# Kernel optimization log

Measured on AMD Instinct MI355X. Metric: run time of the kernel, lower is better.

The kernel has to match this reference:

```python
import jax, jax.numpy as jnp
import numpy as np

NUM_HEADS = 16
CLAMP = 1e4


def setup_inputs() -> dict:
    key = jax.random.key(0)
    ks = jax.random.split(key, 8)
    B, Nq, Nkv, Cq, Ckv = 4, 2048, 2048, 1024, 768
    s_q = 1.0 / np.sqrt(Cq)
    s_kv = 1.0 / np.sqrt(Ckv)
    return {
        "query": jax.random.normal(ks[0], (B, Nq, Cq), jnp.float32),
        "key_value": jax.random.normal(ks[1], (B, Nkv, Ckv), jnp.float32),
        "Wq": jax.random.normal(ks[2], (Cq, Cq), jnp.float32) * s_q,
        "bq": jnp.zeros((Cq,), jnp.float32),
        "Wk": jax.random.normal(ks[3], (Ckv, Cq), jnp.float32) * s_kv,
        "bk": jnp.zeros((Cq,), jnp.float32),
        "Wv": jax.random.normal(ks[4], (Ckv, Cq), jnp.float32) * s_kv,
        "bv": jnp.zeros((Cq,), jnp.float32),
        "Wo": jax.random.normal(ks[5], (Cq, Cq), jnp.float32) * s_q,
        "bo": jnp.zeros((Cq,), jnp.float32),
    }


def reference(query, key_value, Wq, bq, Wk, bk, Wv, bv, Wo, bo):
    B, Nq, Cq = query.shape
    Nkv = key_value.shape[1]
    H = NUM_HEADS
    D = Cq // H
    scale = D ** (-0.5)

    # projections -> [B, H, N, D]
    q = (query @ Wq + bq).reshape(B, Nq, H, D).transpose(0, 2, 1, 3)
    k = (key_value @ Wk + bk).reshape(B, Nkv, H, D).transpose(0, 2, 1, 3)
    v = (key_value @ Wv + bv).reshape(B, Nkv, H, D).transpose(0, 2, 1, 3)

    # scores [B, H, Nq, Nkv] with clamp (mask=None path)
    attn = jnp.einsum("bhqd,bhkd->bhqk", q, k) * scale
    attn = jnp.clip(attn, -CLAMP, CLAMP)
    attn = jax.nn.softmax(attn, axis=-1)
    # NaN fallback: replace with uniform attention if any NaN present
    attn = jnp.where(jnp.any(jnp.isnan(attn)),
                     jnp.asarray(1.0 / Nkv, attn.dtype), attn)

    # weighted sum -> [B, Nq, Cq]
    x = jnp.einsum("bhqk,bhkd->bqhd", attn, v).reshape(B, Nq, Cq)
    return x @ Wo + bo
```

## Files before the change

### kernel.cpp

```cpp
#include <hip/hip_runtime.h>
#include <hip/hip_bf16.h>
#include <stdint.h>


typedef unsigned short u16;
typedef __attribute__((ext_vector_type(4))) short bf16x4;
typedef __attribute__((ext_vector_type(8))) short bf16x8;
typedef __attribute__((ext_vector_type(4))) float f32x4;
typedef __attribute__((ext_vector_type(16))) float f32x16;

__device__ __forceinline__ u16 f2bf(float x) {
  union { float f; uint32_t u; } c; c.f = x;
  uint32_t r = c.u + 0x7fffu + ((c.u >> 16) & 1u);
  return (u16)(r >> 16);
}

__device__ __forceinline__ uint32_t pkbf(float a, float b) {
#if __has_builtin(__builtin_amdgcn_cvt_pk_bf16_f32)
  typedef __attribute__((ext_vector_type(2))) __bf16 bf2;
  bf2 r = __builtin_amdgcn_cvt_pk_bf16_f32(a, b);
  return __builtin_bit_cast(uint32_t, r);
#else
  return (uint32_t)f2bf(a) | ((uint32_t)f2bf(b) << 16);
#endif
}

__device__ __forceinline__ void gld16(const void* g, void* l) {
  __builtin_amdgcn_global_load_lds(
      (const __attribute__((address_space(1))) void*)g,
      (__attribute__((address_space(3))) void*)l, 16, 0, 0);
}

__device__ __forceinline__ void cvt_body(const float* __restrict__ in,
                                         u16* __restrict__ out, int blk) {
  int i = (blk * 256 + threadIdx.x) * 8;
  float4 a = *(const float4*)(in + i);
  float4 b = *(const float4*)(in + i + 4);
  union { u16 u[8]; uint4 v; } o;
  o.u[0] = f2bf(a.x); o.u[1] = f2bf(a.y); o.u[2] = f2bf(a.z); o.u[3] = f2bf(a.w);
  o.u[4] = f2bf(b.x); o.u[5] = f2bf(b.y); o.u[6] = f2bf(b.z); o.u[7] = f2bf(b.w);
  *(uint4*)(out + i) = o.v;
}

__device__ __forceinline__ void transpose_body(const float* __restrict__ in,
                                               u16* __restrict__ out,
                                               int R, int C, int bx, int by) {
  __shared__ float tile[64][65];
  int c0 = bx * 64, r0 = by * 64;
  #pragma unroll
  for (int it = 0; it < 16; it++) {
    int idx = threadIdx.x + it * 256;
    int lr = idx >> 6, lc = idx & 63;
    tile[lr][lc] = in[(size_t)(r0 + lr) * C + c0 + lc];
  }
  __syncthreads();
  #pragma unroll
  for (int it = 0; it < 16; it++) {
    int idx = threadIdx.x + it * 256;
    int lc = idx >> 6, lr = idx & 63;
    out[(size_t)(c0 + lc) * R + r0 + lr] = f2bf(tile[lr][lc]);
  }
}

__global__ void prep_kernel(const float* __restrict__ query,
                            const float* __restrict__ key_value,
                            const float* __restrict__ Wq, const float* __restrict__ Wk,
                            const float* __restrict__ Wv, const float* __restrict__ Wo,
                            u16* qb, u16* kvb, u16* WqT, u16* WkT, u16* WvT, u16* WoT) {
  int blk = blockIdx.x;
  if (blk < 4096) { cvt_body(query, qb, blk); return; }
  if (blk < 7168) { cvt_body(key_value, kvb, blk - 4096); return; }
  if (blk < 7424) { int lo = blk - 7168; transpose_body(Wq, WqT, 1024, 1024, lo & 15, lo >> 4); return; }
  if (blk < 7616) { int lo = blk - 7424; transpose_body(Wk, WkT, 768, 1024, lo & 15, lo >> 4); return; }
  if (blk < 7808) { int lo = blk - 7616; transpose_body(Wv, WvT, 768, 1024, lo & 15, lo >> 4); return; }
  { int lo = blk - 7808; transpose_body(Wo, WoT, 1024, 1024, lo & 15, lo >> 4); return; }
}

template<bool SWAP>
__device__ __forceinline__ void gemm_kloop(const u16* __restrict__ A,
                                           const u16* __restrict__ BT,
                                           int K, char* smem, f32x4 (&acc)[4][4],
                                           int m0, int n0, int tid) {
  const u16* ap[4]; const u16* bp[4]; int ldA[4], ldB[4];
  #pragma unroll
  for (int it2 = 0; it2 < 4; it2++) {
    int s = it2 * 256 + tid;
    int row = s >> 3, cl = (s & 7) ^ (row & 7);
    ap[it2] = A + (size_t)(m0 + row) * K + cl * 8;
    bp[it2] = BT + (size_t)(n0 + row) * K + cl * 8;
    ldA[it2] = s * 16;
    ldB[it2] = 16384 + s * 16;
  }
  const int w = tid >> 6, l = tid & 63;
  const int lm = l & 15, lq = l >> 4;
  const int wr = w >> 1, wc = w & 1;
  int abase[4], bbase[4];
  #pragma unroll
  for (int i = 0; i < 4; i++) {
    int m = wr * 64 + i * 16 + lm;
    abase[i] = m * 128 + ((lq ^ (m & 7)) << 4);
    int n = wc * 64 + i * 16 + lm;
    bbase[i] = 16384 + n * 128 + ((lq ^ (n & 7)) << 4);
  }
  for (int k0 = 0; k0 < K; k0 += 64) {
    #pragma unroll
    for (int it2 = 0; it2 < 4; it2++) {
      gld16(ap[it2], smem + ldA[it2]);
      gld16(bp[it2], smem + ldB[it2]);
      ap[it2] += 64; bp[it2] += 64;
    }
    __syncthreads();
    #pragma unroll
    for (int kk = 0; kk < 2; kk++) {
      bf16x8 af[4], bf[4];
      #pragma unroll
      for (int i = 0; i < 4; i++)
        af[i] = *(const bf16x8*)(smem + (abase[i] ^ (kk << 6)));
      #pragma unroll
      for (int j = 0; j < 4; j++)
        bf[j] = *(const bf16x8*)(smem + (bbase[j] ^ (kk << 6)));
      #pragma unroll
      for (int i = 0; i < 4; i++)
        #pragma unroll
        for (int j = 0; j < 4; j++) {
          if (SWAP)
            acc[i][j] = __builtin_amdgcn_mfma_f32_16x16x32_bf16(bf[j], af[i], acc[i][j], 0, 0, 0);
          else
            acc[i][j] = __builtin_amdgcn_mfma_f32_16x16x32_bf16(af[i], bf[j], acc[i][j], 0, 0, 0);
        }
    }
    __syncthreads();
  }
}

__global__ __launch_bounds__(256, 2)
void gemm_qkv(const u16* __restrict__ qb, const u16* __restrict__ kvb,
              const u16* __restrict__ WqT, const u16* __restrict__ WkT,
              const u16* __restrict__ WvT,
              const float* __restrict__ bq, const float* __restrict__ bk,
              const float* __restrict__ bv,
              u16* __restrict__ Qb, u16* __restrict__ Kbf, u16* __restrict__ Vt,
              float qscale) {
  extern __shared__ __align__(16) char smem[];
  const int tid = threadIdx.x;
  const int w = tid >> 6, l = tid & 63;
  const int lm = l & 15, lq = l >> 4;
  const int m0 = blockIdx.y * 128, n0 = blockIdx.x * 128;
  const int wr = w >> 1, wc = w & 1;
  const int z = blockIdx.z;
  f32x4 acc[4][4] = {};

  u16* etile = (u16*)(smem + w * 9216);
  const int xr = l >> 3, cc = (l & 7) ^ xr;

  if (z < 2) {
    const u16* A = (z == 0) ? qb : kvb;
    const u16* BT = (z == 0) ? WqT : WkT;
    const float* bias = (z == 0) ? bq : bk;
    u16* out = (z == 0) ? Qb : Kbf;
    const float scale = (z == 0) ? qscale : 1.0f;
    const int K = (z == 0) ? 1024 : 768;
    gemm_kloop<true>(A, BT, K, smem, acc, m0, n0, tid);
    #pragma unroll
    for (int j = 0; j < 4; j++) {
      float4 b4 = *(const float4*)&bias[n0 + wc * 64 + j * 16 + lq * 4];
      #pragma unroll
      for (int i = 0; i < 4; i++) {
        uint2 pkd;
        pkd.x = pkbf((acc[i][j][0] + b4.x) * scale, (acc[i][j][1] + b4.y) * scale);
        pkd.y = pkbf((acc[i][j][2] + b4.z) * scale, (acc[i][j][3] + b4.w) * scale);
        *(uint2*)&etile[(i * 16 + lm) * 72 + j * 16 + lq * 4] = pkd;
      }
    }
    u16* gbase = out + (size_t)(m0 + wr * 64) * 1024 + n0 + wc * 64;
    #pragma unroll
    for (int co = 0; co < 8; co++) {
      int ml = co * 8 + xr;
      uint4 d = *(const uint4*)&etile[ml * 72 + cc * 8];
      *(uint4*)&gbase[(size_t)ml * 1024 + cc * 8] = d;
    }
  } else {
    gemm_kloop<false>(kvb, WvT, 768, smem, acc, m0, n0, tid);
    #pragma unroll
    for (int j = 0; j < 4; j++) {
      float bi = bv[n0 + wc * 64 + j * 16 + lm];
      #pragma unroll
      for (int i = 0; i < 4; i++) {
        uint2 pkd;
        pkd.x = pkbf(acc[i][j][0] + bi, acc[i][j][1] + bi);
        pkd.y = pkbf(acc[i][j][2] + bi, acc[i][j][3] + bi);
        *(uint2*)&etile[(j * 16 + lm) * 72 + i * 16 + lq * 4] = pkd;
      }
    }
    const int bb = m0 >> 11, mloc = (m0 & 2047) + wr * 64;
    u16* gbase = Vt + ((size_t)bb * 1024 + n0 + wc * 64) * 2048 + mloc;
    const int kvA = (cc >> 1) * 16 + (cc & 1) * 4;
    #pragma unroll
    for (int co = 0; co < 8; co++) {
      int dl = co * 8 + xr;
      uint2 dA = *(const uint2*)&etile[dl * 72 + kvA];
      uint2 dB = *(const uint2*)&etile[dl * 72 + kvA + 8];
      uint4 d = {dA.x, dA.y, dB.x, dB.y};
      *(uint4*)&gbase[(size_t)dl * 2048 + cc * 8] = d;
    }
  }
}

__global__ __launch_bounds__(256, 2)
void gemm_o(const u16* __restrict__ A, const u16* __restrict__ BT,
            const float* __restrict__ bias, float* __restrict__ Cout) {
  __shared__ __align__(16) char smem[32768];
  const int tid = threadIdx.x;
  const int w = tid >> 6, l = tid & 63;
  const int lm = l & 15, lq = l >> 4;
  const int m0 = blockIdx.y * 128, n0 = blockIdx.x * 128;
  const int wr = w >> 1, wc = w & 1;
  f32x4 acc[4][4] = {};
  gemm_kloop<false>(A, BT, 1024, smem, acc, m0, n0, tid);
  #pragma unroll
  for (int j = 0; j < 4; j++) {
    int gn = n0 + wc * 64 + j * 16 + lm;
    float bi = bias[gn];
    #pragma unroll
    for (int i = 0; i < 4; i++) {
      int gm = m0 + wr * 64 + i * 16 + lq * 4;
      #pragma unroll
      for (int r = 0; r < 4; r++)
        Cout[(size_t)(gm + r) * 1024 + gn] = acc[i][j][r] + bi;
    }
  }
}

__global__ __launch_bounds__(256, 3)
void attn_kernel(const u16* __restrict__ Q, const u16* __restrict__ Kb,
                 const u16* __restrict__ Vt, u16* __restrict__ X) {
  __shared__ __align__(16) char smem[32768];
  const int tid = threadIdx.x, w = tid >> 6, l = tid & 63;
  const int l31 = l & 31, h5 = l >> 5;
  const int bh = blockIdx.x, b = bh >> 4, h = bh & 15;
  const int q0 = blockIdx.y * 128 + w * 32;
  const int rx = l31 & 7;

  const u16* Kg = Kb + (size_t)b * 2048 * 1024 + h * 64;
  const u16* Vg = Vt + (size_t)bh * 64 * 2048;

  const u16 *kp0, *kp1, *vp0, *vp1;
  {
    int s = tid, r = s >> 3, c = (s & 7) ^ (r & 7);
    kp0 = Kg + (size_t)r * 1024 + c * 8;
    vp0 = Vg + (size_t)r * 2048 + c * 8;
    s = 256 + tid; r = s >> 3; c = (s & 7) ^ (r & 7);
    kp1 = Kg + (size_t)r * 1024 + c * 8;
    vp1 = Vg + (size_t)r * 2048 + c * 8;
  }
  const int kd0 = tid * 16, kd1 = (256 + tid) * 16;

  bf16x8 qf[4];
  {
    const u16* qp = Q + ((size_t)(b * 2048 + q0 + l31)) * 1024 + h * 64 + h5 * 8;
    #pragma unroll
    for (int t = 0; t < 4; t++) qf[t] = *(const bf16x8*)(qp + t * 16);
  }

  const int kvb2 = (l31 << 7) | ((rx ^ h5) << 4);
  const int vb2 = 16384 | (l31 << 7) | ((rx ^ h5) << 4);

  f32x16 xacc[2] = {};
  f32x4 ls4 = {0.f, 0.f, 0.f, 0.f};
  const f32x16 KZ = {};

  gld16(kp0, smem + kd0); gld16(kp1, smem + kd1);
  gld16(vp0, smem + 16384 + kd0); gld16(vp1, smem + 16384 + kd1);
  kp0 += 65536; kp1 += 65536; vp0 += 64; vp1 += 64;
  __syncthreads();

#define ATTN_STEP(CUR, DOPREF)                                                  \
  {                                                                             \
    if (DOPREF) {                                                               \
      const int nb = ((CUR) ^ 1) << 13;                                         \
      gld16(kp0, smem + nb + kd0); gld16(kp1, smem + nb + kd1);                 \
      gld16(vp0, smem + 16384 + nb + kd0); gld16(vp1, smem + 16384 + nb + kd1); \
      kp0 += 65536; kp1 += 65536; vp0 += 64; vp1 += 64;                         \
    }                                                                           \
    _Pragma("unroll")                                                           \
    for (int sub = 0; sub < 2; sub++) {                                         \
      const int km = ((CUR) << 13) | (sub << 12);                               \
      bf16x8 kf = *(const bf16x8*)(smem + (kvb2 ^ km));                         \
      f32x16 st = __builtin_amdgcn_mfma_f32_32x32x16_bf16(kf, qf[0], KZ, 0, 0, 0); \
      _Pragma("unroll")                                                         \
      for (int t = 1; t < 4; t++) {                                             \
        kf = *(const bf16x8*)(smem + (kvb2 ^ (km | (t << 5))));                 \
        st = __builtin_amdgcn_mfma_f32_32x32x16_bf16(kf, qf[t], st, 0, 0, 0);   \
      }                                                                         \
      float p[16];                                                              \
      _Pragma("unroll")                                                         \
      for (int r = 0; r < 16; r++) p[r] = __builtin_amdgcn_exp2f(st[r]);        \
      _Pragma("unroll")                                                         \
      for (int u = 0; u < 4; u++)                                               \
        ls4[u] += (p[4 * u] + p[4 * u + 1]) + (p[4 * u + 2] + p[4 * u + 3]);    \
      uint32_t pk[8];                                                           \
      _Pragma("unroll")                                                         \
      for (int qd = 0; qd < 8; qd++) pk[qd] = pkbf(p[2 * qd], p[2 * qd + 1]);   \
      _Pragma("unroll")                                                         \
      for (int c2 = 0; c2 < 2; c2++) {                                          \
        union { uint32_t d[4]; bf16x8 v; } pf;                                  \
        pf.d[0] = pk[4 * c2 + 0]; pf.d[1] = pk[4 * c2 + 1];                     \
        pf.d[2] = pk[4 * c2 + 2]; pf.d[3] = pk[4 * c2 + 3];                     \
        const int vx = ((sub << 2) | (c2 << 1)) << 4;                           \
        _Pragma("unroll")                                                       \
        for (int dt = 0; dt < 2; dt++) {                                        \
          bf16x8 vf = *(const bf16x8*)(smem +                                   \
              (vb2 ^ (((CUR) << 13) | (dt << 12) | vx)));                       \
          xacc[dt] = __builtin_amdgcn_mfma_f32_32x32x16_bf16(vf, pf.v, xacc[dt], 0, 0, 0); \
        }                                                                       \
      }                                                                         \
    }                                                                           \
    __syncthreads();                                                            \
  }

  for (int itp = 0; itp < 15; itp++) {
    ATTN_STEP(0, true)
    ATTN_STEP(1, true)
  }
  ATTN_STEP(0, true)
  ATTN_STEP(1, false)
#undef ATTN_STEP

  float lsum = (ls4[0] + ls4[1]) + (ls4[2] + ls4[3]);
  const float inv = 1.0f / (lsum + __shfl_xor(lsum, 32));
  u16* xp = X + ((size_t)(b * 2048 + q0 + l31)) * 1024 + h * 64;
  #pragma unroll
  for (int dt = 0; dt < 2; dt++)
    #pragma unroll
    for (int g = 0; g < 4; g++) {
      const int d0 = dt * 32 + g * 8 + h5 * 4;
      uint2 o;
      o.x = pkbf(xacc[dt][4 * g + 0] * inv, xacc[dt][4 * g + 1] * inv);
      o.y = pkbf(xacc[dt][4 * g + 2] * inv, xacc[dt][4 * g + 3] * inv);
      *(uint2*)(xp + d0) = o;
    }
}

extern "C" void kernel_launch(void* const* d_in, const int* in_sizes, int n_in,
                              void* d_out, int out_size, void* d_ws, size_t ws_size,
                              hipStream_t stream) {
  const float* query     = (const float*)d_in[0];
  const float* key_value = (const float*)d_in[1];
  const float* Wq = (const float*)d_in[2];
  const float* bq = (const float*)d_in[3];
  const float* Wk = (const float*)d_in[4];
  const float* bk = (const float*)d_in[5];
  const float* Wv = (const float*)d_in[6];
  const float* bv = (const float*)d_in[7];
  const float* Wo = (const float*)d_in[8];
  const float* bo = (const float*)d_in[9];
  float* out = (float*)d_out;

  char* ws = (char*)d_ws;
  size_t off = 0;
  auto alloc = [&](size_t bytes) -> void* {
    void* p = ws + off; off += (bytes + 255) & ~(size_t)255; return p;
  };
  u16* qb  = (u16*)alloc((size_t)8192 * 1024 * 2);
  u16* kvb = (u16*)alloc((size_t)8192 * 768 * 2);
  u16* WqT = (u16*)alloc((size_t)1024 * 1024 * 2);
  u16* WkT = (u16*)alloc((size_t)1024 * 768 * 2);
  u16* WvT = (u16*)alloc((size_t)1024 * 768 * 2);
  u16* WoT = (u16*)alloc((size_t)1024 * 1024 * 2);
  u16* Qb  = (u16*)alloc((size_t)8192 * 1024 * 2);
  u16* Kbf = (u16*)alloc((size_t)8192 * 1024 * 2);
  u16* Vt  = (u16*)alloc((size_t)8192 * 1024 * 2);
  u16* Xb  = (u16*)alloc((size_t)8192 * 1024 * 2);

  prep_kernel<<<8064, 256, 0, stream>>>(query, key_value, Wq, Wk, Wv, Wo,
                                        qb, kvb, WqT, WkT, WvT, WoT);

  const float qscale = 0.125f * 1.4426950408889634f;
  gemm_qkv<<<dim3(8, 64, 3), 256, 36864, stream>>>(qb, kvb, WqT, WkT, WvT,
                                                   bq, bk, bv, Qb, Kbf, Vt, qscale);

  attn_kernel<<<dim3(64, 16), 256, 0, stream>>>(Qb, Kbf, Vt, Xb);

  gemm_o<<<dim3(8, 64), 256, 0, stream>>>(Xb, WoT, bo, out);
}
```

Measured before the change: 293.1 us.

## Process two query tiles per wave in attention to reuse K/V fragments

Each attention wave now handles 64 query rows, as two 32-row tiles, instead of 32. K and V fragments loaded from LDS are reused across both tiles, and the grid is halved. This cuts LDS and global K/V traffic per query and gives more independent MFMA work to interleave. The cost is higher register pressure, so attention occupancy drops to 2 blocks per CU while the GEMM kernels' launch bounds are raised to 3.

Measured after the change: 291.0 us. No clear change (-0.7%).

```diff
diff --git a/kernel.cpp b/kernel.cpp
--- a/kernel.cpp
+++ b/kernel.cpp
@@ -4,6 +4,7 @@
 
 
 typedef unsigned short u16;
+typedef __attribute__((ext_vector_type(2))) float f32x2;
 typedef __attribute__((ext_vector_type(4))) short bf16x4;
 typedef __attribute__((ext_vector_type(8))) short bf16x8;
 typedef __attribute__((ext_vector_type(4))) float f32x4;
@@ -133,7 +134,7 @@
   }
 }
 
-__global__ __launch_bounds__(256, 2)
+__global__ __launch_bounds__(256, 3)
 void gemm_qkv(const u16* __restrict__ qb, const u16* __restrict__ kvb,
               const u16* __restrict__ WqT, const u16* __restrict__ WkT,
               const u16* __restrict__ WvT,
@@ -206,7 +207,7 @@
   }
 }
 
-__global__ __launch_bounds__(256, 2)
+__global__ __launch_bounds__(256, 3)
 void gemm_o(const u16* __restrict__ A, const u16* __restrict__ BT,
             const float* __restrict__ bias, float* __restrict__ Cout) {
   __shared__ __align__(16) char smem[32768];
@@ -231,14 +232,14 @@
   }
 }
 
-__global__ __launch_bounds__(256, 3)
+__global__ __launch_bounds__(256, 2)
 void attn_kernel(const u16* __restrict__ Q, const u16* __restrict__ Kb,
                  const u16* __restrict__ Vt, u16* __restrict__ X) {
   __shared__ __align__(16) char smem[32768];
   const int tid = threadIdx.x, w = tid >> 6, l = tid & 63;
   const int l31 = l & 31, h5 = l >> 5;
   const int bh = blockIdx.x, b = bh >> 4, h = bh & 15;
-  const int q0 = blockIdx.y * 128 + w * 32;
+  const int q0 = blockIdx.y * 256 + w * 64;
   const int rx = l31 & 7;
 
   const u16* Kg = Kb + (size_t)b * 2048 * 1024 + h * 64;
@@ -255,18 +256,21 @@
   }
   const int kd0 = tid * 16, kd1 = (256 + tid) * 16;
 
-  bf16x8 qf[4];
+  bf16x8 qfA[4], qfB[4];
   {
     const u16* qp = Q + ((size_t)(b * 2048 + q0 + l31)) * 1024 + h * 64 + h5 * 8;
     #pragma unroll
-    for (int t = 0; t < 4; t++) qf[t] = *(const bf16x8*)(qp + t * 16);
+    for (int t = 0; t < 4; t++) qfA[t] = *(const bf16x8*)(qp + t * 16);
+    qp += (size_t)32 * 1024;
+    #pragma unroll
+    for (int t = 0; t < 4; t++) qfB[t] = *(const bf16x8*)(qp + t * 16);
   }
 
   const int kvb2 = (l31 << 7) | ((rx ^ h5) << 4);
   const int vb2 = 16384 | (l31 << 7) | ((rx ^ h5) << 4);
 
-  f32x16 xacc[2] = {};
-  f32x4 ls4 = {0.f, 0.f, 0.f, 0.f};
+  f32x16 xaccA[2] = {}, xaccB[2] = {};
+  f32x2 lsA = {0.f, 0.f}, lsB = {0.f, 0.f};
   const f32x16 KZ = {};
 
   gld16(kp0, smem + kd0); gld16(kp1, smem + kd1);
@@ -285,33 +289,51 @@
     _Pragma("unroll")                                                           \
     for (int sub = 0; sub < 2; sub++) {                                         \
       const int km = ((CUR) << 13) | (sub << 12);                               \
-      bf16x8 kf = *(const bf16x8*)(smem + (kvb2 ^ km));                         \
-      f32x16 st = __builtin_amdgcn_mfma_f32_32x32x16_bf16(kf, qf[0], KZ, 0, 0, 0); \
-      _Pragma("unroll")                                                         \
-      for (int t = 1; t < 4; t++) {                                             \
-        kf = *(const bf16x8*)(smem + (kvb2 ^ (km | (t << 5))));                 \
-        st = __builtin_amdgcn_mfma_f32_32x32x16_bf16(kf, qf[t], st, 0, 0, 0);   \
+      bf16x8 kf[4];                                                             \
+      _Pragma("unroll")                                                         \
+      for (int t = 0; t < 4; t++)                                               \
+        kf[t] = *(const bf16x8*)(smem + (kvb2 ^ (km | (t << 5))));              \
+      f32x16 st = __builtin_amdgcn_mfma_f32_32x32x16_bf16(kf[0], qfA[0], KZ, 0, 0, 0); \
+      _Pragma("unroll")                                                         \
+      for (int t = 1; t < 4; t++)                                               \
+        st = __builtin_amdgcn_mfma_f32_32x32x16_bf16(kf[t], qfA[t], st, 0, 0, 0); \
+      uint32_t pkA[8], pkB[8];                                                  \
+      _Pragma("unroll")                                                         \
+      for (int u = 0; u < 4; u++) {                                             \
+        float p0 = __builtin_amdgcn_exp2f(st[4 * u + 0]);                       \
+        float p1 = __builtin_amdgcn_exp2f(st[4 * u + 1]);                       \
+        float p2 = __builtin_amdgcn_exp2f(st[4 * u + 2]);                       \
+        float p3 = __builtin_amdgcn_exp2f(st[4 * u + 3]);                       \
+        lsA += (f32x2){p0 + p2, p1 + p3};                                       \
+        pkA[2 * u] = pkbf(p0, p1); pkA[2 * u + 1] = pkbf(p2, p3);               \
       }                                                                         \
-      float p[16];                                                              \
-      _Pragma("unroll")                                                         \
-      for (int r = 0; r < 16; r++) p[r] = __builtin_amdgcn_exp2f(st[r]);        \
-      _Pragma("unroll")                                                         \
-      for (int u = 0; u < 4; u++)                                               \
-        ls4[u] += (p[4 * u] + p[4 * u + 1]) + (p[4 * u + 2] + p[4 * u + 3]);    \
-      uint32_t pk[8];                                                           \
-      _Pragma("unroll")                                                         \
-      for (int qd = 0; qd < 8; qd++) pk[qd] = pkbf(p[2 * qd], p[2 * qd + 1]);   \
+      st = __builtin_amdgcn_mfma_f32_32x32x16_bf16(kf[0], qfB[0], KZ, 0, 0, 0); \
+      _Pragma("unroll")                                                         \
+      for (int t = 1; t < 4; t++)                                               \
+        st = __builtin_amdgcn_mfma_f32_32x32x16_bf16(kf[t], qfB[t], st, 0, 0, 0); \
+      _Pragma("unroll")                                                         \
+      for (int u = 0; u < 4; u++) {                                             \
+        float p0 = __builtin_amdgcn_exp2f(st[4 * u + 0]);                       \
+        float p1 = __builtin_amdgcn_exp2f(st[4 * u + 1]);                       \
+        float p2 = __builtin_amdgcn_exp2f(st[4 * u + 2]);                       \
+        float p3 = __builtin_amdgcn_exp2f(st[4 * u + 3]);                       \
+        lsB += (f32x2){p0 + p2, p1 + p3};                                       \
+        pkB[2 * u] = pkbf(p0, p1); pkB[2 * u + 1] = pkbf(p2, p3);               \
+      }                                                                         \
       _Pragma("unroll")                                                         \
       for (int c2 = 0; c2 < 2; c2++) {                                          \
-        union { uint32_t d[4]; bf16x8 v; } pf;                                  \
-        pf.d[0] = pk[4 * c2 + 0]; pf.d[1] = pk[4 * c2 + 1];                     \
-        pf.d[2] = pk[4 * c2 + 2]; pf.d[3] = pk[4 * c2 + 3];                     \
+        union { uint32_t d[4]; bf16x8 v; } pfA, pfB;                            \
+        _Pragma("unroll")                                                       \
+        for (int dd = 0; dd < 4; dd++) {                                        \
+          pfA.d[dd] = pkA[4 * c2 + dd]; pfB.d[dd] = pkB[4 * c2 + dd];           \
+        }                                                                       \
         const int vx = ((sub << 2) | (c2 << 1)) << 4;                           \
         _Pragma("unroll")                                                       \
         for (int dt = 0; dt < 2; dt++) {                                        \
           bf16x8 vf = *(const bf16x8*)(smem +                                   \
               (vb2 ^ (((CUR) << 13) | (dt << 12) | vx)));                       \
-          xacc[dt] = __builtin_amdgcn_mfma_f32_32x32x16_bf16(vf, pf.v, xacc[dt], 0, 0, 0); \
+          xaccA[dt] = __builtin_amdgcn_mfma_f32_32x32x16_bf16(vf, pfA.v, xaccA[dt], 0, 0, 0); \
+          xaccB[dt] = __builtin_amdgcn_mfma_f32_32x32x16_bf16(vf, pfB.v, xaccB[dt], 0, 0, 0); \
         }                                                                       \
       }                                                                         \
     }                                                                           \
@@ -326,19 +348,36 @@
   ATTN_STEP(1, false)
 #undef ATTN_STEP
 
-  float lsum = (ls4[0] + ls4[1]) + (ls4[2] + ls4[3]);
-  const float inv = 1.0f / (lsum + __shfl_xor(lsum, 32));
-  u16* xp = X + ((size_t)(b * 2048 + q0 + l31)) * 1024 + h * 64;
-  #pragma unroll
-  for (int dt = 0; dt < 2; dt++)
-    #pragma unroll
-    for (int g = 0; g < 4; g++) {
-      const int d0 = dt * 32 + g * 8 + h5 * 4;
-      uint2 o;
-      o.x = pkbf(xacc[dt][4 * g + 0] * inv, xacc[dt][4 * g + 1] * inv);
-      o.y = pkbf(xacc[dt][4 * g + 2] * inv, xacc[dt][4 * g + 3] * inv);
-      *(uint2*)(xp + d0) = o;
-    }
+  {
+    float lsum = lsA[0] + lsA[1];
+    const float inv = 1.0f / (lsum + __shfl_xor(lsum, 32));
+    u16* xp = X + ((size_t)(b * 2048 + q0 + l31)) * 1024 + h * 64;
+    #pragma unroll
+    for (int dt = 0; dt < 2; dt++)
+      #pragma unroll
+      for (int g = 0; g < 4; g++) {
+        const int d0 = dt * 32 + g * 8 + h5 * 4;
+        uint2 o;
+        o.x = pkbf(xaccA[dt][4 * g + 0] * inv, xaccA[dt][4 * g + 1] * inv);
+        o.y = pkbf(xaccA[dt][4 * g + 2] * inv, xaccA[dt][4 * g + 3] * inv);
+        *(uint2*)(xp + d0) = o;
+      }
+  }
+  {
+    float lsum = lsB[0] + lsB[1];
+    const float inv = 1.0f / (lsum + __shfl_xor(lsum, 32));
+    u16* xp = X + ((size_t)(b * 2048 + q0 + 32 + l31)) * 1024 + h * 64;
+    #pragma unroll
+    for (int dt = 0; dt < 2; dt++)
+      #pragma unroll
+      for (int g = 0; g < 4; g++) {
+        const int d0 = dt * 32 + g * 8 + h5 * 4;
+        uint2 o;
+        o.x = pkbf(xaccB[dt][4 * g + 0] * inv, xaccB[dt][4 * g + 1] * inv);
+        o.y = pkbf(xaccB[dt][4 * g + 2] * inv, xaccB[dt][4 * g + 3] * inv);
+        *(uint2*)(xp + d0) = o;
+      }
+  }
 }
 
 extern "C" void kernel_launch(void* const* d_in, const int* in_sizes, int n_in,
@@ -379,7 +418,7 @@
   gemm_qkv<<<dim3(8, 64, 3), 256, 36864, stream>>>(qb, kvb, WqT, WkT, WvT,
                                                    bq, bk, bv, Qb, Kbf, Vt, qscale);
 
-  attn_kernel<<<dim3(64, 16), 256, 0, stream>>>(Qb, Kbf, Vt, Xb);
+  attn_kernel<<<dim3(64, 8), 256, 0, stream>>>(Qb, Kbf, Vt, Xb);
 
   gemm_o<<<dim3(8, 64), 256, 0, stream>>>(Xb, WoT, bo, out);
 }
```
